# Performance work log

Hardware: AMD Instinct MI355X
Metric: run time of the kernel (lower is better)

## Reference

```python
import jax, jax.numpy as jnp
import numpy as np

KERNEL = 31
PAD = 15
SMOOTHNESS = 1.0


def _avg_pool2d_31(x):
    # x: [B, 1, H, W]; torch avg_pool2d default count_include_pad=True ->
    # divide by full window size (31*31) everywhere, zeros in the padding.
    s = jax.lax.reduce_window(
        x, 0.0, jax.lax.add,
        window_dimensions=(1, 1, KERNEL, KERNEL),
        window_strides=(1, 1, 1, 1),
        padding=((0, 0), (0, 0), (PAD, PAD), (PAD, PAD)))
    return s / (KERNEL * KERNEL)


def setup_inputs() -> dict:
    key = jax.random.key(0)
    k1, k2 = jax.random.split(key)
    pred = jax.random.normal(k1, (16, 2, 512, 512), dtype=jnp.float32)
    mask = jax.random.randint(k2, (16, 512, 512), 0, 2, dtype=jnp.int64)
    return {"pred": pred, "mask": mask}


def reference(pred, mask):
    # mask[mask == 255] = 0
    mask = jnp.where(mask == 255, 0, mask)
    mask_f = mask.astype(pred.dtype)                         # [B,H,W]

    pooled = _avg_pool2d_31(mask_f[:, None])[:, 0]           # [B,H,W]
    weit = 1.0 + 5.0 * jnp.abs(pooled - mask_f)              # [B,H,W]

    # cross_entropy(reduction='none'); ignore_index=255 never fires since
    # 255 was already remapped to 0 above.
    logp = jax.nn.log_softmax(pred, axis=1)                  # [B,2,H,W]
    wbce = -jnp.take_along_axis(logp, mask[:, None], axis=1)[:, 0]  # [B,H,W]

    weit_sum = weit.sum(axis=(1, 2))
    wbce = (weit * wbce).sum(axis=(1, 2)) / weit_sum         # [B]

    p1 = jnp.exp(logp[:, 1])                                 # softmax(pred)[:,1]
    inter = (p1 * mask_f * weit).sum(axis=(1, 2))
    cardinality = ((p1 + mask_f) * weit).sum(axis=(1, 2))
    union = cardinality - inter
    wiou = 1.0 - (inter + SMOOTHNESS) / (union + SMOOTHNESS)

    return (wbce + wiou).mean()
```

## Files before the change

### kernel.cpp

```cpp
#include <hip/hip_runtime.h>

constexpr int Bn = 16;
constexpr int Hn = 512;
constexpr int Wn = 512;
constexpr int PADR = 15;
constexpr float INV_KK = 1.0f / (31.0f * 31.0f);
constexpr int RPW = 2;
constexpr int WPB = 4;
constexpr int RPB = RPW * WPB;
constexpr int BPB = Hn / RPB;

__global__ void pack_kernel(const int* __restrict__ mask,
                            unsigned char* __restrict__ mask8) {
    const size_t i = (size_t)blockIdx.x * 256 + threadIdx.x;
    const int4 mm = reinterpret_cast<const int4*>(mask)[i];
    uchar4 r;
    r.x = (mm.x == 255) ? 0 : (unsigned char)mm.x;
    r.y = (mm.y == 255) ? 0 : (unsigned char)mm.y;
    r.z = (mm.z == 255) ? 0 : (unsigned char)mm.z;
    r.w = (mm.w == 255) ? 0 : (unsigned char)mm.w;
    reinterpret_cast<uchar4*>(mask8)[i] = r;
}

__global__ void fused_kernel(const float* __restrict__ pred,
                             const unsigned char* __restrict__ mask8,
                             float* __restrict__ part) {
    const int t = threadIdx.x;
    const int lane = t & 63;
    const int wv = t >> 6;
    const int b = blockIdx.y;
    const int h0 = blockIdx.x * RPB;
    const int r0 = h0 + wv * RPW;
    const int c0 = lane * 8;

    const unsigned char* mb = mask8 + (size_t)b * Hn * Wn;
    const float* pb = pred + (size_t)b * 2 * Hn * Wn;
    const float* pb1 = pb + (size_t)Hn * Wn;

    unsigned int e0 = 0, o0 = 0, e1 = 0, o1 = 0;
    {
        const int glo = (r0 - PADR < 0) ? 0 : r0 - PADR;
        const int ghi = (r0 + PADR > Hn - 1) ? Hn - 1 : r0 + PADR;
        for (int g = glo; g <= ghi; ++g) {
            const uint2 x = *reinterpret_cast<const uint2*>(mb + (size_t)g * Wn + c0);
            e0 += x.x & 0x00FF00FFu; o0 += (x.x >> 8) & 0x00FF00FFu;
            e1 += x.y & 0x00FF00FFu; o1 += (x.y >> 8) & 0x00FF00FFu;
        }
    }

    float a_weit = 0.f, a_wbce = 0.f, a_inter = 0.f, a_card = 0.f;

#pragma unroll
    for (int rr = 0; rr < RPW; ++rr) {
        const int r = r0 + rr;

        float q[8];
        q[0] = (float)(e0 & 0xFFFFu);
        q[1] = q[0] + (float)(o0 & 0xFFFFu);
        q[2] = q[1] + (float)(e0 >> 16);
        q[3] = q[2] + (float)(o0 >> 16);
        q[4] = q[3] + (float)(e1 & 0xFFFFu);
        q[5] = q[4] + (float)(o1 & 0xFFFFu);
        q[6] = q[5] + (float)(e1 >> 16);
        q[7] = q[6] + (float)(o1 >> 16);

        float s = q[7];
#pragma unroll
        for (int off = 1; off < 64; off <<= 1) {
            const float n = __shfl_up(s, off, 64);
            if (lane >= off) s += n;
        }
        const float pre = s - q[7];
        float P[8];
#pragma unroll
        for (int k = 0; k < 8; ++k) P[k] = pre + q[k];
        const float total = __shfl(P[7], 63, 64);

        const int sl = (lane - 2 < 0) ? 0 : lane - 2;
        const int s1 = (lane + 1 > 63) ? 63 : lane + 1;
        const int s2 = (lane + 2 > 63) ? 63 : lane + 2;
        float plo[8], phi[8];
#pragma unroll
        for (int k = 0; k < 8; ++k) plo[k] = __shfl(P[k], sl, 64);
        phi[0] = __shfl(P[7], s1, 64);
#pragma unroll
        for (int k = 1; k < 8; ++k) phi[k] = __shfl(P[k - 1], s2, 64);

        const uint2 mm = *reinterpret_cast<const uint2*>(mb + (size_t)r * Wn + c0);
        const float4 qa0 = *reinterpret_cast<const float4*>(pb + (size_t)r * Wn + c0);
        const float4 qa1 = *reinterpret_cast<const float4*>(pb + (size_t)r * Wn + c0 + 4);
        const float4 qb0 = *reinterpret_cast<const float4*>(pb1 + (size_t)r * Wn + c0);
        const float4 qb1 = *reinterpret_cast<const float4*>(pb1 + (size_t)r * Wn + c0 + 4);
        const float pA[8] = {qa0.x, qa0.y, qa0.z, qa0.w, qa1.x, qa1.y, qa1.z, qa1.w};
        const float pB[8] = {qb0.x, qb0.y, qb0.z, qb0.w, qb1.x, qb1.y, qb1.z, qb1.w};

#pragma unroll
        for (int k = 0; k < 8; ++k) {
            const int i = c0 + k;
            const unsigned int mwrd = (k < 4) ? mm.x : mm.y;
            const int m = (mwrd >> (8 * (k & 3))) & 0xFF;
            const float mf = (float)m;
            const float p0 = pA[k];
            const float p1 = pB[k];

            const float lo_v = (i >= PADR + 1) ? plo[k] : 0.0f;
            const float hi_v = (i + PADR <= Wn - 1) ? phi[k] : total;
            const float pooled = (hi_v - lo_v) * INV_KK;

            const float mx = fmaxf(p0, p1);
            const float lse = mx + __logf(__expf(p0 - mx) + __expf(p1 - mx));
            const float lp0 = p0 - lse;
            const float lp1 = p1 - lse;

            const float wbce = m ? -lp1 : -lp0;
            const float p1s = __expf(lp1);

            const float weit = 1.0f + 5.0f * fabsf(pooled - mf);
            a_weit += weit;
            a_wbce += weit * wbce;
            a_inter += p1s * mf * weit;
            a_card += (p1s + mf) * weit;
        }

        if (rr + 1 < RPW) {
            const int ga = r + 1 + PADR;
            const int gs = r - PADR;
            if (ga < Hn) {
                const uint2 x = *reinterpret_cast<const uint2*>(mb + (size_t)ga * Wn + c0);
                e0 += x.x & 0x00FF00FFu; o0 += (x.x >> 8) & 0x00FF00FFu;
                e1 += x.y & 0x00FF00FFu; o1 += (x.y >> 8) & 0x00FF00FFu;
            }
            if (gs >= 0) {
                const uint2 x = *reinterpret_cast<const uint2*>(mb + (size_t)gs * Wn + c0);
                e0 -= x.x & 0x00FF00FFu; o0 -= (x.x >> 8) & 0x00FF00FFu;
                e1 -= x.y & 0x00FF00FFu; o1 -= (x.y >> 8) & 0x00FF00FFu;
            }
        }
    }

    __shared__ float red[4][4];
#pragma unroll
    for (int off = 32; off > 0; off >>= 1) {
        a_weit += __shfl_down(a_weit, off, 64);
        a_wbce += __shfl_down(a_wbce, off, 64);
        a_inter += __shfl_down(a_inter, off, 64);
        a_card += __shfl_down(a_card, off, 64);
    }
    if (lane == 0) {
        red[wv][0] = a_weit;
        red[wv][1] = a_wbce;
        red[wv][2] = a_inter;
        red[wv][3] = a_card;
    }
    __syncthreads();
    if (t < 4) {
        part[((size_t)b * BPB + blockIdx.x) * 4 + t] =
            red[0][t] + red[1][t] + red[2][t] + red[3][t];
    }
}

__global__ void __launch_bounds__(1024)
reduce_finalize_kernel(const float* __restrict__ part, float* __restrict__ out) {
    const int t = threadIdx.x;
    const int b = t >> 6;
    const int l = t & 63;

    float a0 = 0.f, a1 = 0.f, a2 = 0.f, a3 = 0.f;
    for (int j = l; j < BPB; j += 64) {
        const float4 v = *reinterpret_cast<const float4*>(part + ((size_t)b * BPB + j) * 4);
        a0 += v.x; a1 += v.y; a2 += v.z; a3 += v.w;
    }
#pragma unroll
    for (int off = 32; off > 0; off >>= 1) {
        a0 += __shfl_down(a0, off, 64);
        a1 += __shfl_down(a1, off, 64);
        a2 += __shfl_down(a2, off, 64);
        a3 += __shfl_down(a3, off, 64);
    }

    __shared__ float loss[Bn];
    if (l == 0) {
        const float wbce = a1 / a0;
        const float uni = a3 - a2;
        const float wiou = 1.0f - (a2 + 1.0f) / (uni + 1.0f);
        loss[b] = wbce + wiou;
    }
    __syncthreads();
    if (t == 0) {
        float s = 0.0f;
#pragma unroll
        for (int k = 0; k < Bn; ++k) s += loss[k];
        out[0] = s * (1.0f / (float)Bn);
    }
}

extern "C" void kernel_launch(void* const* d_in, const int* in_sizes, int n_in,
                              void* d_out, int out_size, void* d_ws, size_t ws_size,
                              hipStream_t stream) {
    const float* pred = (const float*)d_in[0];
    const int* mask = (const int*)d_in[1];
    unsigned char* mask8 = (unsigned char*)d_ws;
    float* part = (float*)(mask8 + (size_t)Bn * Hn * Wn);
    float* out = (float*)d_out;

    hipLaunchKernelGGL(pack_kernel, dim3(Bn * Hn * Wn / 4 / 256), dim3(256),
                       0, stream, mask, mask8);
    hipLaunchKernelGGL(fused_kernel, dim3(BPB, Bn), dim3(256), 0, stream,
                       pred, mask8, part);
    hipLaunchKernelGGL(reduce_finalize_kernel, dim3(1), dim3(1024), 0, stream,
                       part, out);
}
```

Before: 28.47 us.

## Precompute horizontal box sums in pack kernel, vertical sliding sum in fused kernel

The pack kernel now also computes each row's 31-wide horizontal window sum with a wave prefix scan and stores it as a byte array. The fused kernel then slides vertically over these horizontal sums, so it no longer runs a prefix scan and neighbour shuffles per output row. Both kernels use a 1D grid whose block-to-(batch, row group) mapping interleaves batches, likely aimed at locality across XCDs. The cost is an extra byte-sized intermediate that must be written and read back, and the scan work moves into the pack stage rather than disappearing.

After: 25.94 us. 1.1x faster.

```diff
diff --git a/kernel.cpp b/kernel.cpp
--- a/kernel.cpp
+++ b/kernel.cpp
@@ -5,34 +5,94 @@
 constexpr int Wn = 512;
 constexpr int PADR = 15;
 constexpr float INV_KK = 1.0f / (31.0f * 31.0f);
-constexpr int RPW = 2;
-constexpr int WPB = 4;
-constexpr int RPB = RPW * WPB;
-constexpr int BPB = Hn / RPB;
-
-__global__ void pack_kernel(const int* __restrict__ mask,
-                            unsigned char* __restrict__ mask8) {
-    const size_t i = (size_t)blockIdx.x * 256 + threadIdx.x;
-    const int4 mm = reinterpret_cast<const int4*>(mask)[i];
-    uchar4 r;
-    r.x = (mm.x == 255) ? 0 : (unsigned char)mm.x;
-    r.y = (mm.y == 255) ? 0 : (unsigned char)mm.y;
-    r.z = (mm.z == 255) ? 0 : (unsigned char)mm.z;
-    r.w = (mm.w == 255) ? 0 : (unsigned char)mm.w;
-    reinterpret_cast<uchar4*>(mask8)[i] = r;
+
+__device__ __forceinline__ void decode_fid(int fid, int& b, int& grp) {
+    b = (fid & 7) * 2 + ((fid >> 3) & 1);
+    grp = fid >> 4;
+}
+
+__global__ void pack_hbox_kernel(const int* __restrict__ mask,
+                                 unsigned char* __restrict__ mask8,
+                                 unsigned char* __restrict__ hsum8) {
+    int b, grp;
+    decode_fid(blockIdx.x, b, grp);
+    const int lane = threadIdx.x & 63;
+    const int wv = threadIdx.x >> 6;
+    const int c0 = lane * 8;
+
+    const int* mb = mask + (size_t)b * Hn * Wn;
+    unsigned char* m8 = mask8 + (size_t)b * Hn * Wn;
+    unsigned char* h8 = hsum8 + (size_t)b * Hn * Wn;
+
+#pragma unroll
+    for (int rr = 0; rr < 2; ++rr) {
+        const int r = grp * 8 + wv * 2 + rr;
+        const int4 a = *reinterpret_cast<const int4*>(mb + (size_t)r * Wn + c0);
+        const int4 c = *reinterpret_cast<const int4*>(mb + (size_t)r * Wn + c0 + 4);
+        const int mv[8] = {a.x, a.y, a.z, a.w, c.x, c.y, c.z, c.w};
+
+        unsigned int w0 = 0, w1 = 0;
+        float q[8];
+        float run = 0.0f;
+#pragma unroll
+        for (int k = 0; k < 8; ++k) {
+            const int m = (mv[k] == 255) ? 0 : mv[k];
+            if (k < 4) w0 |= (unsigned int)m << (8 * k);
+            else       w1 |= (unsigned int)m << (8 * (k - 4));
+            run += (float)m;
+            q[k] = run;
+        }
+        *reinterpret_cast<uint2*>(m8 + (size_t)r * Wn + c0) = make_uint2(w0, w1);
+
+        float s = q[7];
+#pragma unroll
+        for (int off = 1; off < 64; off <<= 1) {
+            const float n = __shfl_up(s, off, 64);
+            if (lane >= off) s += n;
+        }
+        const float pre = s - q[7];
+        float P[8];
+#pragma unroll
+        for (int k = 0; k < 8; ++k) P[k] = pre + q[k];
+        const float total = __shfl(P[7], 63, 64);
+
+        const int sl = (lane < 2) ? 0 : lane - 2;
+        const int s1 = (lane > 62) ? 63 : lane + 1;
+        const int s2 = (lane > 61) ? 63 : lane + 2;
+        float plo[8], phi[8];
+#pragma unroll
+        for (int k = 0; k < 8; ++k) plo[k] = __shfl(P[k], sl, 64);
+        phi[0] = __shfl(P[7], s1, 64);
+#pragma unroll
+        for (int k = 1; k < 8; ++k) phi[k] = __shfl(P[k - 1], s2, 64);
+
+        unsigned int h0w = 0, h1w = 0;
+#pragma unroll
+        for (int k = 0; k < 8; ++k) {
+            const int i = c0 + k;
+            const float lo = (i >= PADR + 1) ? plo[k] : 0.0f;
+            const float hi = (i + PADR <= Wn - 1) ? phi[k] : total;
+            const unsigned int hv = (unsigned int)(hi - lo);
+            if (k < 4) h0w |= hv << (8 * k);
+            else       h1w |= hv << (8 * (k - 4));
+        }
+        *reinterpret_cast<uint2*>(h8 + (size_t)r * Wn + c0) = make_uint2(h0w, h1w);
+    }
 }
 
 __global__ void fused_kernel(const float* __restrict__ pred,
                              const unsigned char* __restrict__ mask8,
+                             const unsigned char* __restrict__ hsum8,
                              float* __restrict__ part) {
+    int b, bx;
+    decode_fid(blockIdx.x, b, bx);
     const int t = threadIdx.x;
     const int lane = t & 63;
     const int wv = t >> 6;
-    const int b = blockIdx.y;
-    const int h0 = blockIdx.x * RPB;
-    const int r0 = h0 + wv * RPW;
+    const int r0 = bx * 8 + wv * 2;
     const int c0 = lane * 8;
 
+    const unsigned char* hb = hsum8 + (size_t)b * Hn * Wn;
     const unsigned char* mb = mask8 + (size_t)b * Hn * Wn;
     const float* pb = pred + (size_t)b * 2 * Hn * Wn;
     const float* pb1 = pb + (size_t)Hn * Wn;
@@ -42,7 +102,7 @@
         const int glo = (r0 - PADR < 0) ? 0 : r0 - PADR;
         const int ghi = (r0 + PADR > Hn - 1) ? Hn - 1 : r0 + PADR;
         for (int g = glo; g <= ghi; ++g) {
-            const uint2 x = *reinterpret_cast<const uint2*>(mb + (size_t)g * Wn + c0);
+            const uint2 x = *reinterpret_cast<const uint2*>(hb + (size_t)g * Wn + c0);
             e0 += x.x & 0x00FF00FFu; o0 += (x.x >> 8) & 0x00FF00FFu;
             e1 += x.y & 0x00FF00FFu; o1 += (x.y >> 8) & 0x00FF00FFu;
         }
@@ -51,40 +111,14 @@
     float a_weit = 0.f, a_wbce = 0.f, a_inter = 0.f, a_card = 0.f;
 
 #pragma unroll
-    for (int rr = 0; rr < RPW; ++rr) {
+    for (int rr = 0; rr < 2; ++rr) {
         const int r = r0 + rr;
 
-        float q[8];
-        q[0] = (float)(e0 & 0xFFFFu);
-        q[1] = q[0] + (float)(o0 & 0xFFFFu);
-        q[2] = q[1] + (float)(e0 >> 16);
-        q[3] = q[2] + (float)(o0 >> 16);
-        q[4] = q[3] + (float)(e1 & 0xFFFFu);
-        q[5] = q[4] + (float)(o1 & 0xFFFFu);
-        q[6] = q[5] + (float)(e1 >> 16);
-        q[7] = q[6] + (float)(o1 >> 16);
-
-        float s = q[7];
-#pragma unroll
-        for (int off = 1; off < 64; off <<= 1) {
-            const float n = __shfl_up(s, off, 64);
-            if (lane >= off) s += n;
-        }
-        const float pre = s - q[7];
-        float P[8];
-#pragma unroll
-        for (int k = 0; k < 8; ++k) P[k] = pre + q[k];
-        const float total = __shfl(P[7], 63, 64);
-
-        const int sl = (lane - 2 < 0) ? 0 : lane - 2;
-        const int s1 = (lane + 1 > 63) ? 63 : lane + 1;
-        const int s2 = (lane + 2 > 63) ? 63 : lane + 2;
-        float plo[8], phi[8];
-#pragma unroll
-        for (int k = 0; k < 8; ++k) plo[k] = __shfl(P[k], sl, 64);
-        phi[0] = __shfl(P[7], s1, 64);
-#pragma unroll
-        for (int k = 1; k < 8; ++k) phi[k] = __shfl(P[k - 1], s2, 64);
+        const float vs[8] = {
+            (float)(e0 & 0xFFFFu), (float)(o0 & 0xFFFFu),
+            (float)(e0 >> 16),     (float)(o0 >> 16),
+            (float)(e1 & 0xFFFFu), (float)(o1 & 0xFFFFu),
+            (float)(e1 >> 16),     (float)(o1 >> 16)};
 
         const uint2 mm = *reinterpret_cast<const uint2*>(mb + (size_t)r * Wn + c0);
         const float4 qa0 = *reinterpret_cast<const float4*>(pb + (size_t)r * Wn + c0);
@@ -96,16 +130,13 @@
 
 #pragma unroll
         for (int k = 0; k < 8; ++k) {
-            const int i = c0 + k;
             const unsigned int mwrd = (k < 4) ? mm.x : mm.y;
             const int m = (mwrd >> (8 * (k & 3))) & 0xFF;
             const float mf = (float)m;
             const float p0 = pA[k];
             const float p1 = pB[k];
 
-            const float lo_v = (i >= PADR + 1) ? plo[k] : 0.0f;
-            const float hi_v = (i + PADR <= Wn - 1) ? phi[k] : total;
-            const float pooled = (hi_v - lo_v) * INV_KK;
+            const float pooled = vs[k] * INV_KK;
 
             const float mx = fmaxf(p0, p1);
             const float lse = mx + __logf(__expf(p0 - mx) + __expf(p1 - mx));
@@ -122,16 +153,16 @@
             a_card += (p1s + mf) * weit;
         }
 
-        if (rr + 1 < RPW) {
+        if (rr == 0) {
             const int ga = r + 1 + PADR;
             const int gs = r - PADR;
             if (ga < Hn) {
-                const uint2 x = *reinterpret_cast<const uint2*>(mb + (size_t)ga * Wn + c0);
+                const uint2 x = *reinterpret_cast<const uint2*>(hb + (size_t)ga * Wn + c0);
                 e0 += x.x & 0x00FF00FFu; o0 += (x.x >> 8) & 0x00FF00FFu;
                 e1 += x.y & 0x00FF00FFu; o1 += (x.y >> 8) & 0x00FF00FFu;
             }
             if (gs >= 0) {
-                const uint2 x = *reinterpret_cast<const uint2*>(mb + (size_t)gs * Wn + c0);
+                const uint2 x = *reinterpret_cast<const uint2*>(hb + (size_t)gs * Wn + c0);
                 e0 -= x.x & 0x00FF00FFu; o0 -= (x.x >> 8) & 0x00FF00FFu;
                 e1 -= x.y & 0x00FF00FFu; o1 -= (x.y >> 8) & 0x00FF00FFu;
             }
@@ -154,7 +185,7 @@
     }
     __syncthreads();
     if (t < 4) {
-        part[((size_t)b * BPB + blockIdx.x) * 4 + t] =
+        part[((size_t)b * 64 + bx) * 4 + t] =
             red[0][t] + red[1][t] + red[2][t] + red[3][t];
     }
 }
@@ -166,8 +197,8 @@
     const int l = t & 63;
 
     float a0 = 0.f, a1 = 0.f, a2 = 0.f, a3 = 0.f;
-    for (int j = l; j < BPB; j += 64) {
-        const float4 v = *reinterpret_cast<const float4*>(part + ((size_t)b * BPB + j) * 4);
+    for (int j = l; j < 64; j += 64) {
+        const float4 v = *reinterpret_cast<const float4*>(part + ((size_t)b * 64 + j) * 4);
         a0 += v.x; a1 += v.y; a2 += v.z; a3 += v.w;
     }
 #pragma unroll
@@ -200,13 +231,14 @@
     const float* pred = (const float*)d_in[0];
     const int* mask = (const int*)d_in[1];
     unsigned char* mask8 = (unsigned char*)d_ws;
-    float* part = (float*)(mask8 + (size_t)Bn * Hn * Wn);
+    unsigned char* hsum8 = mask8 + (size_t)Bn * Hn * Wn;
+    float* part = (float*)(hsum8 + (size_t)Bn * Hn * Wn);
     float* out = (float*)d_out;
 
-    hipLaunchKernelGGL(pack_kernel, dim3(Bn * Hn * Wn / 4 / 256), dim3(256),
-                       0, stream, mask, mask8);
-    hipLaunchKernelGGL(fused_kernel, dim3(BPB, Bn), dim3(256), 0, stream,
-                       pred, mask8, part);
+    hipLaunchKernelGGL(pack_hbox_kernel, dim3(1024), dim3(256), 0, stream,
+                       mask, mask8, hsum8);
+    hipLaunchKernelGGL(fused_kernel, dim3(1024), dim3(256), 0, stream,
+                       pred, mask8, hsum8, part);
     hipLaunchKernelGGL(reduce_finalize_kernel, dim3(1), dim3(1024), 0, stream,
                        part, out);
 }
```
